# Kernel optimization log

Hardware: AMD Instinct MI355X
Metric: run time of the kernel (lower is better)

## Reference

```python
import jax, jax.numpy as jnp
import numpy as np

EMB = 1024
HEADS = 16
HEAD_DIM = EMB // HEADS
B, S = 4, 2048


def setup_inputs() -> dict:
    key = jax.random.key(0)
    ks = jax.random.split(key, 7)
    sc = 1.0 / np.sqrt(EMB)
    return {
        "query": jax.random.normal(ks[0], (B, S, EMB), jnp.float32),
        "key": jax.random.normal(ks[1], (B, S, EMB), jnp.float32),
        "value": jax.random.normal(ks[2], (B, S, EMB), jnp.float32),
        "Wq": jax.random.normal(ks[3], (EMB, EMB), jnp.float32) * sc,
        "Wk": jax.random.normal(ks[4], (EMB, EMB), jnp.float32) * sc,
        "Wv": jax.random.normal(ks[5], (EMB, EMB), jnp.float32) * sc,
        "Wo": jax.random.normal(ks[6], (EMB, EMB), jnp.float32) * sc,
    }


def reference(query, key, value, Wq, Wk, Wv, Wo):
    # nn.Linear applies x @ W^T; W stored as [out, in]
    def split_heads(x):  # [B,S,E] -> [B,H,S,D]
        return x.reshape(B, -1, HEADS, HEAD_DIM).transpose(0, 2, 1, 3)

    q = split_heads(query @ Wq.T)
    k = split_heads(key @ Wk.T)
    v = split_heads(value @ Wv.T)
    scores = jnp.einsum('bhse,bhte->bhst', q, k) / np.sqrt(HEAD_DIM).astype(np.float32)
    attn = jax.nn.softmax(scores, axis=-1)
    ctx = jnp.einsum('bhst,bhtd->bshd', attn, v)  # [B,S,H,D]
    out = ctx.reshape(B, -1, EMB) @ Wo.T
    return out
```

## Files before the change

kernel.cpp:

```cpp
#include <hip/hip_runtime.h>
#include <hip/hip_bf16.h>

#define EMB   1024
#define HEADS 16
#define HDIM  64
#define BB    4
#define SS    2048
#define MROWS (BB*SS)

typedef __bf16 bf16_t;
typedef __bf16 bf16x4_t __attribute__((ext_vector_type(4)));
typedef __bf16 bf16x8   __attribute__((ext_vector_type(8)));
typedef float  f32x4    __attribute__((ext_vector_type(4)));

__device__ __forceinline__ void glds16(const void* g, void* l) {
  __builtin_amdgcn_global_load_lds(
      (const __attribute__((address_space(1))) void*)g,
      (__attribute__((address_space(3))) void*)l, 16, 0, 0);
}

__launch_bounds__(256)
__global__ void cast_w(const float* s0, const float* s1, const float* s2,
                       const float* s3,
                       bf16_t* d0, bf16_t* d1, bf16_t* d2, bf16_t* d3) {
  const int z = blockIdx.z;
  const float* ss[4] = {s0, s1, s2, s3};
  bf16_t*      dd[4] = {d0, d1, d2, d3};
  const float* s = ss[z];
  bf16_t*      d = dd[z];
  const int i = (blockIdx.x*256 + threadIdx.x) * 8;
  const f32x4 a = *(const f32x4*)&s[i];
  const f32x4 b = *(const f32x4*)&s[i+4];
  bf16x8 r;
  r[0]=(bf16_t)a[0]; r[1]=(bf16_t)a[1]; r[2]=(bf16_t)a[2]; r[3]=(bf16_t)a[3];
  r[4]=(bf16_t)b[0]; r[5]=(bf16_t)b[1]; r[6]=(bf16_t)b[2]; r[7]=(bf16_t)b[3];
  *(bf16x8*)&d[i] = r;
}

__launch_bounds__(256, 4)
__global__ void gemm_qkv(const float* A0, const float* A1, const float* A2,
                         const bf16_t* W0, const bf16_t* W1, const bf16_t* W2,
                         bf16_t* C0, bf16_t* C1, bf16_t* C2, float sscale) {
  __shared__ __align__(16) bf16_t As[2][4096];
  __shared__ __align__(16) bf16_t Bs[2][4096];
  const int tid  = threadIdx.x;
  const int wave = tid >> 6, lane = tid & 63;
  const int quad = lane >> 4, l16 = lane & 15;
  const int wm = wave >> 1, wn = wave & 1;

  const int fid = blockIdx.x + 8*(blockIdx.y + 64*blockIdx.z);
  const int xcd = fid & 7, s = fid >> 3;
  const int bn0 = (s & 7) * 128;
  const int p   = xcd + 8*(s >> 3);
  const int z   = p >> 6;
  const int bm0 = (p & 63) * 128;

  const float*  A = (z == 0) ? A0 : (z == 1) ? A1 : A2;
  const bf16_t* W = (z == 0) ? W0 : (z == 1) ? W1 : W2;
  bf16_t*       C = (z == 0) ? C0 : (z == 1) ? C1 : C2;
  const float oscale = (z == 0) ? sscale : 1.0f;

  const int arow  = tid >> 1;
  const int acolh = (tid & 1) * 16;
  const float* Arow = A + (size_t)(bm0 + arow)*EMB + acolh;

  f32x4 acc[4][4] = {};
  f32x4 ar[4];

  auto loadA = [&](int k0) {
#pragma unroll
    for (int j = 0; j < 4; ++j)
      ar[j] = *(const f32x4*)&Arow[k0 + j*4];
  };
  auto writeA = [&](int bf) {
    bf16x8 h0, h1;
#pragma unroll
    for (int r = 0; r < 4; ++r) {
      h0[r] = (bf16_t)ar[0][r];  h0[4+r] = (bf16_t)ar[1][r];
      h1[r] = (bf16_t)ar[2][r];  h1[4+r] = (bf16_t)ar[3][r];
    }
    *(bf16x8*)&As[bf][arow*32 + acolh]     = h0;
    *(bf16x8*)&As[bf][arow*32 + acolh + 8] = h1;
  };
  auto stageW = [&](int k0, int bf) {
#pragma unroll
    for (int j = 0; j < 2; ++j) {
      const int i   = wave*2 + j;
      const int row = i*16 + (lane >> 2);
      const int col = (lane & 3) * 8;
      glds16(W + (size_t)(bn0 + row)*EMB + k0 + col, &Bs[bf][i*512]);
    }
  };
  auto compute = [&](int bf) {
    bf16x8 a[4], b[4];
#pragma unroll
    for (int t2 = 0; t2 < 4; ++t2) {
      a[t2] = *(const bf16x8*)&As[bf][(wm*64 + t2*16 + l16)*32 + quad*8];
      b[t2] = *(const bf16x8*)&Bs[bf][(wn*64 + t2*16 + l16)*32 + quad*8];
    }
#pragma unroll
    for (int mt = 0; mt < 4; ++mt)
#pragma unroll
      for (int nt = 0; nt < 4; ++nt)
        acc[mt][nt] = __builtin_amdgcn_mfma_f32_16x16x32_bf16(a[mt], b[nt], acc[mt][nt], 0, 0, 0);
  };

  loadA(0);
  stageW(0, 0);
  writeA(0);
  __syncthreads();

  const int NK = EMB / 32;
  for (int t = 0; t < NK; ++t) {
    const int cur = t & 1;
    if (t + 1 < NK) {
      loadA((t + 1) * 32);
      stageW((t + 1) * 32, cur ^ 1);
    }
    compute(cur);
    if (t + 1 < NK) writeA(cur ^ 1);
    __syncthreads();
  }

  if (z == 2) {
    const int bb = bm0 >> 11;
    const int T  = ((bm0 & 2047) >> 6) + wm;
    const int h  = (bn0 >> 6) + wn;
    bf16_t* base = C + ((size_t)(bb*HEADS + h)*32 + T)*4096;
#pragma unroll
    for (int ks = 0; ks < 2; ++ks)
#pragma unroll
      for (int nt = 0; nt < 4; ++nt) {
        bf16x8 v;
#pragma unroll
        for (int r = 0; r < 4; ++r) {
          v[r]     = (bf16_t)acc[2*ks][nt][r];
          v[4 + r] = (bf16_t)acc[2*ks + 1][nt][r];
        }
        *(bf16x8*)&base[((nt*2 + ks)*64 + quad*16 + l16)*8] = v;
      }
  } else {
#pragma unroll
    for (int mt = 0; mt < 4; ++mt) {
      const int row = bm0 + wm*64 + mt*16 + quad*4;
#pragma unroll
      for (int nt = 0; nt < 4; ++nt) {
        const int col = bn0 + wn*64 + nt*16 + l16;
#pragma unroll
        for (int r = 0; r < 4; ++r)
          C[(size_t)(row + r)*EMB + col] = (bf16_t)(acc[mt][nt][r] * oscale);
      }
    }
  }
}

__device__ __forceinline__ void gemm_core(const bf16_t* __restrict__ A,
                                          const bf16_t* __restrict__ W,
                                          bf16_t* As, bf16_t* Bs,
                                          f32x4 acc[4][4],
                                          int bm0, int bn0,
                                          int wave, int lane) {
  const int quad = lane >> 4, l16 = lane & 15;
  const int wm = wave >> 1, wn = wave & 1;
  for (int k0 = 0; k0 < EMB; k0 += 32) {
#pragma unroll
    for (int j = 0; j < 2; ++j) {
      const int i   = wave*2 + j;
      const int row = i*16 + (lane >> 2);
      const int col = (lane & 3) * 8;
      glds16(A + (size_t)(bm0 + row)*EMB + k0 + col, &As[i*512]);
      glds16(W + (size_t)(bn0 + row)*EMB + k0 + col, &Bs[i*512]);
    }
    __syncthreads();

    bf16x8 a[4], b[4];
#pragma unroll
    for (int t = 0; t < 4; ++t) {
      a[t] = *(const bf16x8*)&As[(wm*64 + t*16 + l16)*32 + quad*8];
      b[t] = *(const bf16x8*)&Bs[(wn*64 + t*16 + l16)*32 + quad*8];
    }
#pragma unroll
    for (int mt = 0; mt < 4; ++mt)
#pragma unroll
      for (int nt = 0; nt < 4; ++nt)
        acc[mt][nt] = __builtin_amdgcn_mfma_f32_16x16x32_bf16(a[mt], b[nt], acc[mt][nt], 0, 0, 0);
    __syncthreads();
  }
}

__launch_bounds__(256)
__global__ void gemm_out(const bf16_t* __restrict__ A, const bf16_t* __restrict__ W,
                         float* __restrict__ C) {
  __shared__ __align__(16) bf16_t As[128*32];
  __shared__ __align__(16) bf16_t Bs[128*32];
  const int tid  = threadIdx.x;
  const int wave = tid >> 6, lane = tid & 63;
  const int quad = lane >> 4, l16 = lane & 15;
  const int wm = wave >> 1, wn = wave & 1;

  const int fid = blockIdx.x + 8*blockIdx.y;
  const int xcd = fid & 7, s = fid >> 3;
  const int bn0 = (s & 7) * 128;
  const int bm0 = (xcd*8 + (s >> 3)) * 128;

  f32x4 acc[4][4] = {};
  gemm_core(A, W, As, Bs, acc, bm0, bn0, wave, lane);

#pragma unroll
  for (int mt = 0; mt < 4; ++mt) {
    const int row = bm0 + wm*64 + mt*16 + quad*4;
#pragma unroll
    for (int nt = 0; nt < 4; ++nt) {
      const int col = bn0 + wn*64 + nt*16 + l16;
#pragma unroll
      for (int r = 0; r < 4; ++r)
        C[(size_t)(row + r)*EMB + col] = acc[mt][nt][r];
    }
  }
}

__launch_bounds__(512, 8)
__global__ void attn(const bf16_t* Qp, const bf16_t* __restrict__ Kp,
                     const bf16_t* __restrict__ Vt, bf16_t* Cx) {
  __shared__ __align__(16) bf16_t Ks[2][4096];
  __shared__ __align__(16) bf16_t Vs[2][4096];

  const int tid  = threadIdx.x;
  const int wave = tid >> 6, lane = tid & 63;
  const int quad = lane >> 4, l16 = lane & 15;

  const int fid  = blockIdx.x + 16*(blockIdx.y + 16*blockIdx.z);
  const int xcd  = fid & 7, s = fid >> 3;
  const int q0   = (s & 15) * 128;
  const int pair = xcd*8 + (s >> 4);
  const int h    = pair & 15;
  const int b    = pair >> 4;

  bf16x8 qf[2];
  {
    const size_t qr = (size_t)(b*SS + q0 + wave*16 + l16)*EMB + h*HDIM;
    qf[0] = *(const bf16x8*)&Qp[qr + quad*8];
    qf[1] = *(const bf16x8*)&Qp[qr + 32 + quad*8];
  }

  const bf16_t* Kb = Kp + (size_t)b*SS*EMB + h*HDIM;
  const bf16_t* Vb = Vt + ((size_t)(b*HEADS + h)*32)*4096;

  f32x4 o[4] = {};
  f32x4 lsv = {};

  auto stage = [&](int ti, int bf) {
    const int t0 = ti * 64;
    const int i  = wave;
    glds16(Kb + (size_t)(t0 + (i&3)*16 + l16)*EMB + (i>>2)*32 + quad*8,
           &Ks[bf][i*512]);
    glds16(Vb + (size_t)ti*4096 + i*512 + lane*8, &Vs[bf][i*512]);
  };

  stage(0, 0);

  const int NT = SS / 64;
  for (int t = 0, buf = 0; t < NT; ++t, buf ^= 1) {
    __syncthreads();
    if (t + 1 < NT) stage(t + 1, buf ^ 1);

    f32x4 st[4] = {};
#pragma unroll
    for (int cb = 0; cb < 4; ++cb) {
      const bf16x8 kf0 = *(const bf16x8*)&Ks[buf][cb*512 + lane*8];
      const bf16x8 kf1 = *(const bf16x8*)&Ks[buf][2048 + cb*512 + lane*8];
      st[cb] = __builtin_amdgcn_mfma_f32_16x16x32_bf16(kf0, qf[0], st[cb], 0, 0, 0);
      st[cb] = __builtin_amdgcn_mfma_f32_16x16x32_bf16(kf1, qf[1], st[cb], 0, 0, 0);
    }

#pragma unroll
    for (int kb = 0; kb < 4; ++kb) {
#pragma unroll
      for (int r = 0; r < 4; ++r)
        st[kb][r] = __builtin_amdgcn_exp2f(st[kb][r]);
      lsv += st[kb];
    }
    bf16x8 pb[2];
#pragma unroll
    for (int ks = 0; ks < 2; ++ks)
#pragma unroll
      for (int r = 0; r < 4; ++r) {
        pb[ks][r]     = (bf16_t)st[2*ks][r];
        pb[ks][4 + r] = (bf16_t)st[2*ks + 1][r];
      }

#pragma unroll
    for (int ks = 0; ks < 2; ++ks)
#pragma unroll
      for (int dt = 0; dt < 4; ++dt) {
        const bf16x8 vf = *(const bf16x8*)&Vs[buf][((dt*2 + ks)*64 + lane)*8];
        o[dt] = __builtin_amdgcn_mfma_f32_16x16x32_bf16(vf, pb[ks], o[dt], 0, 0, 0);
      }
  }

  float l = lsv[0] + lsv[1] + lsv[2] + lsv[3];
  l += __shfl_xor(l, 16, 64);
  l += __shfl_xor(l, 32, 64);
  const float inv = 1.0f / l;
  const size_t row = (size_t)(b*SS + q0 + wave*16 + l16)*EMB + h*HDIM;
#pragma unroll
  for (int dt = 0; dt < 4; ++dt) {
    bf16x4_t v;
#pragma unroll
    for (int r = 0; r < 4; ++r) v[r] = (bf16_t)(o[dt][r] * inv);
    *(bf16x4_t*)&Cx[row + dt*16 + quad*4] = v;
  }
}

extern "C" void kernel_launch(void* const* d_in, const int* in_sizes, int n_in,
                              void* d_out, int out_size, void* d_ws, size_t ws_size,
                              hipStream_t stream) {
  (void)in_sizes; (void)n_in; (void)out_size; (void)ws_size;
  const float* query = (const float*)d_in[0];
  const float* key   = (const float*)d_in[1];
  const float* value = (const float*)d_in[2];
  const float* WqF   = (const float*)d_in[3];
  const float* WkF   = (const float*)d_in[4];
  const float* WvF   = (const float*)d_in[5];
  const float* WoF   = (const float*)d_in[6];

  const size_t AN = (size_t)MROWS*EMB;
  const size_t WN = (size_t)EMB*EMB;
  float* out = (float*)d_out;
  bf16_t* S5 = (bf16_t*)d_out;
  bf16_t* S6 = S5 + AN;

  bf16_t* S2  = (bf16_t*)d_ws;
  bf16_t* Wqb = S2 + AN;
  bf16_t* Wkb = Wqb + WN;
  bf16_t* Wvb = Wkb + WN;
  bf16_t* Wob = Wvb + WN;

  const float sscale = 0.125f * 1.44269504f;

  const dim3 gw  (512, 1, 4);
  const dim3 gqkv(EMB/128, MROWS/128, 3);
  const dim3 gg  (EMB/128, MROWS/128);
  const dim3 gattn(SS/128, HEADS, BB);

  cast_w<<<gw, 256, 0, stream>>>(WqF, WkF, WvF, WoF, Wqb, Wkb, Wvb, Wob);
  gemm_qkv<<<gqkv, 256, 0, stream>>>(query, key, value, Wqb, Wkb, Wvb,
                                     S2, S6, S5, sscale);
  attn<<<gattn, 512, 0, stream>>>(S2, S6, S5, S2);
  gemm_out<<<gg, 256, 0, stream>>>(S2, Wob, out);
}
```

Baseline: 345.0 us.

## Stage fp32 A tiles via direct global-to-LDS loads, drop double buffering in QKV GEMM

```diff
diff --git a/kernel.cpp b/kernel.cpp
--- a/kernel.cpp
+++ b/kernel.cpp
@@ -37,12 +37,12 @@
   *(bf16x8*)&d[i] = r;
 }
 
-__launch_bounds__(256, 4)
+__launch_bounds__(256)
 __global__ void gemm_qkv(const float* A0, const float* A1, const float* A2,
                          const bf16_t* W0, const bf16_t* W1, const bf16_t* W2,
                          bf16_t* C0, bf16_t* C1, bf16_t* C2, float sscale) {
-  __shared__ __align__(16) bf16_t As[2][4096];
-  __shared__ __align__(16) bf16_t Bs[2][4096];
+  __shared__ __align__(16) float  Asf[4096];
+  __shared__ __align__(16) bf16_t Bs[4096];
   const int tid  = threadIdx.x;
   const int wave = tid >> 6, lane = tid & 63;
   const int quad = lane >> 4, l16 = lane & 15;
@@ -60,65 +60,45 @@
   bf16_t*       C = (z == 0) ? C0 : (z == 1) ? C1 : C2;
   const float oscale = (z == 0) ? sscale : 1.0f;
 
-  const int arow  = tid >> 1;
-  const int acolh = (tid & 1) * 16;
-  const float* Arow = A + (size_t)(bm0 + arow)*EMB + acolh;
-
+  const int arow = lane >> 3;
+  const int aslt = (lane & 7) ^ arow;
   f32x4 acc[4][4] = {};
-  f32x4 ar[4];
-
-  auto loadA = [&](int k0) {
-#pragma unroll
-    for (int j = 0; j < 4; ++j)
-      ar[j] = *(const f32x4*)&Arow[k0 + j*4];
-  };
-  auto writeA = [&](int bf) {
-    bf16x8 h0, h1;
-#pragma unroll
-    for (int r = 0; r < 4; ++r) {
-      h0[r] = (bf16_t)ar[0][r];  h0[4+r] = (bf16_t)ar[1][r];
-      h1[r] = (bf16_t)ar[2][r];  h1[4+r] = (bf16_t)ar[3][r];
-    }
-    *(bf16x8*)&As[bf][arow*32 + acolh]     = h0;
-    *(bf16x8*)&As[bf][arow*32 + acolh + 8] = h1;
-  };
-  auto stageW = [&](int k0, int bf) {
+
+  for (int k0 = 0; k0 < EMB; k0 += 32) {
+#pragma unroll
+    for (int c = 0; c < 4; ++c) {
+      const int i = wave*4 + c;
+      glds16(A + (size_t)(bm0 + i*8 + arow)*EMB + k0 + aslt*4,
+             &Asf[i*256]);
+    }
 #pragma unroll
     for (int j = 0; j < 2; ++j) {
       const int i   = wave*2 + j;
       const int row = i*16 + (lane >> 2);
       const int col = (lane & 3) * 8;
-      glds16(W + (size_t)(bn0 + row)*EMB + k0 + col, &Bs[bf][i*512]);
-    }
-  };
-  auto compute = [&](int bf) {
+      glds16(W + (size_t)(bn0 + row)*EMB + k0 + col, &Bs[i*512]);
+    }
+    __syncthreads();
+
     bf16x8 a[4], b[4];
 #pragma unroll
     for (int t2 = 0; t2 < 4; ++t2) {
-      a[t2] = *(const bf16x8*)&As[bf][(wm*64 + t2*16 + l16)*32 + quad*8];
-      b[t2] = *(const bf16x8*)&Bs[bf][(wn*64 + t2*16 + l16)*32 + quad*8];
+      const int rl = wm*64 + t2*16 + l16;
+      const float* Ab = &Asf[(rl >> 3)*256 + (rl & 7)*32];
+      const f32x4 v0 = *(const f32x4*)&Ab[(((quad*2)    ) ^ (rl & 7))*4];
+      const f32x4 v1 = *(const f32x4*)&Ab[(((quad*2) + 1) ^ (rl & 7))*4];
+#pragma unroll
+      for (int r = 0; r < 4; ++r) {
+        a[t2][r]     = (bf16_t)v0[r];
+        a[t2][4 + r] = (bf16_t)v1[r];
+      }
+      b[t2] = *(const bf16x8*)&Bs[(wn*64 + t2*16 + l16)*32 + quad*8];
     }
 #pragma unroll
     for (int mt = 0; mt < 4; ++mt)
 #pragma unroll
       for (int nt = 0; nt < 4; ++nt)
         acc[mt][nt] = __builtin_amdgcn_mfma_f32_16x16x32_bf16(a[mt], b[nt], acc[mt][nt], 0, 0, 0);
-  };
-
-  loadA(0);
-  stageW(0, 0);
-  writeA(0);
-  __syncthreads();
-
-  const int NK = EMB / 32;
-  for (int t = 0; t < NK; ++t) {
-    const int cur = t & 1;
-    if (t + 1 < NK) {
-      loadA((t + 1) * 32);
-      stageW((t + 1) * 32, cur ^ 1);
-    }
-    compute(cur);
-    if (t + 1 < NK) writeA(cur ^ 1);
     __syncthreads();
   }
 
```

Result: no change. 344.1 us (-0.3%).
